# Optimization experiments

Measured on AMD Instinct MI355X. Metric: run time of the kernel, lower is better.

## Reference

```python
import jax, jax.numpy as jnp
import numpy as np

# (multiplicity, dim=2l+1) per irreducible field, for both input and output
RS = [(8, 1), (8, 3), (8, 5)]
SIZE = 3          # conv kernel spatial size
B_EL = 2          # radial basis elements per (i,j) kernel block
EPS = 1e-5


def _se3_bn_conv(x, weight, bases):
    """Training-mode SE3BatchNorm stats fused into dynamic kernel build + conv3d.
    x: (B, C_in, D, H, W); weight: flat (sum mi*mj*b_el,);
    bases[i][j]: (b_el, di, dj, SIZE, SIZE, SIZE).
    """
    B = x.shape[0]
    means = []    # per scalar (d==1) field: (m,)
    scales = []   # per field: (m,) inverse-std factors
    ix = 0
    for m, d in RS:
        field = x[:, ix:ix + m * d].reshape(B, m, d, -1)
        ix += m * d
        if d == 1:
            mean = jax.lax.stop_gradient(field.mean(axis=-1).mean(axis=0).reshape(-1))
            field = field - mean.reshape(1, m, 1, 1)
            means.append(mean)
        # reduce='mean': sum over d, mean over spatial, mean over batch (detached)
        norm = jax.lax.stop_gradient(jnp.sum(field * field, axis=2).mean(axis=-1).mean(axis=0))
        scales.append((norm + EPS) ** -0.5)

    # Build normalized dynamic kernel blocks and compensating bias
    widx = 0
    row_blocks = []
    bias_parts = []
    for i, (mi, di) in enumerate(RS):
        col_blocks = []
        bia = jnp.zeros((mi * di,), x.dtype)
        imean = 0
        for j, (mj, dj) in enumerate(RS):
            basis = bases[i][j]                     # (b, di, dj, s, s, s)
            b = basis.shape[0]
            w = weight[widx:widx + mi * mj * b].reshape(mi, mj, b)
            widx += mi * mj * b
            w = w * scales[j][None, :, None]        # per-input-field BN rescale
            # block: (mi*di, mj*dj, s, s, s)
            block = jnp.einsum('uvb,bdexyz->udvexyz', w, basis)
            col_blocks.append(block.reshape(mi * di, mj * dj, SIZE, SIZE, SIZE))
            if di == 1 and dj == 1:
                mean = means[imean]
                imean += 1
                identity = basis.reshape(b, -1).sum(-1)         # (b,)
                corr = (w.reshape(-1, b) @ identity[:, None]).reshape(mi, mj)
                bia = bia - (corr @ mean[:, None]).reshape(-1)
        row_blocks.append(jnp.concatenate(col_blocks, axis=1))
        bias_parts.append(bia)
    kernel = jnp.concatenate(row_blocks, axis=0)    # (C_out, C_in, s, s, s)
    bias = jnp.concatenate(bias_parts)              # (C_out,)

    out = jax.lax.conv_general_dilated(
        x, kernel, window_strides=(1, 1, 1), padding='VALID',
        dimension_numbers=('NCDHW', 'OIDHW', 'NCDHW'))
    return out + bias[None, :, None, None, None]


def setup_inputs() -> dict:
    key = jax.random.key(0)
    k_x, k_w = jax.random.split(key)
    C = sum(m * d for m, d in RS)  # 72
    x = jax.random.normal(k_x, (8, C, 32, 32, 32), jnp.float32)
    total_w = sum(mi * mj * B_EL for mi, _ in RS for mj, _ in RS)  # 1152
    weight = jax.random.normal(k_w, (total_w,), jnp.float32) * 0.1
    inp = {'x': x, 'weight': weight}
    for i, (mi, di) in enumerate(RS):
        for j, (mj, dj) in enumerate(RS):
            kb = jax.random.fold_in(key, 100 + 10 * i + j)
            inp['basis_{}_{}'.format(i, j)] = jax.random.normal(
                kb, (B_EL, di, dj, SIZE, SIZE, SIZE), jnp.float32) / (SIZE ** 1.5)
    return inp


def reference(x, weight, basis_0_0, basis_0_1, basis_0_2,
              basis_1_0, basis_1_1, basis_1_2,
              basis_2_0, basis_2_1, basis_2_2):
    bases = [[basis_0_0, basis_0_1, basis_0_2],
             [basis_1_0, basis_1_1, basis_1_2],
             [basis_2_0, basis_2_1, basis_2_2]]
    return _se3_bn_conv(x, weight, bases)
```

## Files before the change

kernel.cpp:

```cpp
#include <hip/hip_runtime.h>
#include <hip/hip_fp16.h>
#include <math.h>

#define NCH 72
#define SP  32768
#define NBATCH 8
#define NTOT (NBATCH*SP)

#define WS_SUMX   0
#define WS_SUMSQ  72
#define WS_SCALE  144
#define WS_BIAS   216
#define WS_K      288

#define WS_XH_BYTES 323712
#define XH_ROW   2720
#define XH_PLANE 87040
#define XH_BATCH 2785280

typedef __attribute__((ext_vector_type(8))) _Float16 half8;
typedef __attribute__((ext_vector_type(4))) float float4v;
typedef __attribute__((ext_vector_type(4))) int int4v;

__device__ __forceinline__ void chmap(int c, int& f, int& m, int& d, int& dim) {
  if (c < 8)       { f = 0; m = c;          d = 0;          dim = 1; }
  else if (c < 32) { f = 1; m = (c - 8)/3;  d = (c - 8)%3;  dim = 3; }
  else             { f = 2; m = (c - 32)/5; d = (c - 32)%5; dim = 5; }
}

__global__ __launch_bounds__(256) void prepack_kernel(const float* __restrict__ x,
                                                      float* __restrict__ ws) {
  __shared__ __align__(16) short tile[256 * 88];
  __shared__ float segS[72][3], segQ[72][3];
  const int t    = threadIdx.x;
  const int z    = blockIdx.x >> 1;
  const int half = blockIdx.x & 1;
  const int b    = blockIdx.y;
  ushort* xh = (ushort*)((char*)ws + WS_XH_BYTES);
  const float* xb = x + (size_t)b * NCH * SP + z * 1024 + half * 512;

  const int ci_s = t % 72, seg = t / 72;
  float accS = 0.f, accQ = 0.f;

  *(int4v*)&tile[t * 88 + 72] = (int4v){0, 0, 0, 0};

  for (int c = 0; c < 2; ++c) {
    if (c) __syncthreads();
    #pragma unroll
    for (int cig = 0; cig < 18; ++cig) {
      float v0 = xb[(size_t)(cig*4 + 0) * SP + c * 256 + t];
      float v1 = xb[(size_t)(cig*4 + 1) * SP + c * 256 + t];
      float v2 = xb[(size_t)(cig*4 + 2) * SP + c * 256 + t];
      float v3 = xb[(size_t)(cig*4 + 3) * SP + c * 256 + t];
      short s4[4] = { (short)__half_as_short(__float2half(v0)),
                      (short)__half_as_short(__float2half(v1)),
                      (short)__half_as_short(__float2half(v2)),
                      (short)__half_as_short(__float2half(v3)) };
      *(int2*)&tile[t * 88 + cig * 4] = *(const int2*)s4;
    }
    __syncthreads();
    {
      ushort* gb = xh + (size_t)b * XH_BATCH + (size_t)(z * 32 + (half * 2 + c) * 8) * XH_ROW;
      #pragma unroll
      for (int j = 0; j < 10; ++j) {
        const int s   = t + j * 256;
        const int pos = s / 10, part = s - pos * 10;
        const int4v v = *(const int4v*)&tile[pos * 88 + part * 8];
        const int row = pos >> 5, xx = pos & 31;
        *(int4v*)(gb + (size_t)row * XH_ROW + xx * 80 + part * 8) = v;
      }
    }
    if (seg < 3) {
      const int p0 = seg * 86;
      const int pn = (seg == 2) ? 84 : 86;
      for (int i = 0; i < pn; ++i) {
        const float v = __half2float(__short_as_half(tile[(p0 + i) * 88 + ci_s]));
        accS += v; accQ += v * v;
      }
    }
  }
  if (seg < 3) { segS[ci_s][seg] = accS; segQ[ci_s][seg] = accQ; }
  __syncthreads();
  if (t < 144) {
    const int which = t / 72, ci = t % 72;
    const float v = which ? (segQ[ci][0] + segQ[ci][1] + segQ[ci][2])
                          : (segS[ci][0] + segS[ci][1] + segS[ci][2]);
    atomicAdd(&ws[(which ? WS_SUMSQ : WS_SUMX) + ci], v);
  }
}

__global__ __launch_bounds__(128) void finalize_kernel(const float* __restrict__ weight,
                                                       const float* __restrict__ basis00,
                                                       float* __restrict__ ws) {
  __shared__ float s_mean[8], s_scale[8];
  const int c = threadIdx.x;
  const float invN = 1.0f / (float)NTOT;
  if (c < NCH) {
    float norm;
    if (c < 8) {
      float m = ws[WS_SUMX + c] * invN;
      norm = ws[WS_SUMSQ + c] * invN - m * m;
      s_mean[c] = m;
    } else if (c < 32) {
      int m0 = 8 + ((c - 8) / 3) * 3;
      norm = (ws[WS_SUMSQ+m0] + ws[WS_SUMSQ+m0+1] + ws[WS_SUMSQ+m0+2]) * invN;
    } else {
      int m0 = 32 + ((c - 32) / 5) * 5;
      norm = (ws[WS_SUMSQ+m0] + ws[WS_SUMSQ+m0+1] + ws[WS_SUMSQ+m0+2]
            + ws[WS_SUMSQ+m0+3] + ws[WS_SUMSQ+m0+4]) * invN;
    }
    float sc = 1.0f / sqrtf(norm + 1e-5f);
    ws[WS_SCALE + c] = sc;
    if (c < 8) s_scale[c] = sc;
  }
  __syncthreads();
  if (c < NCH) {
    float bia = 0.f;
    if (c < 8) {
      float id0 = 0.f, id1 = 0.f;
      #pragma unroll
      for (int t = 0; t < 27; ++t) { id0 += basis00[t]; id1 += basis00[27 + t]; }
      #pragma unroll
      for (int v = 0; v < 8; ++v) {
        float s  = s_scale[v];
        float w0 = weight[(c*8 + v)*2 + 0] * s;
        float w1 = weight[(c*8 + v)*2 + 1] * s;
        bia -= (w0 * id0 + w1 * id1) * s_mean[v];
      }
    }
    ws[WS_BIAS + c] = bia;
  }
}

__global__ __launch_bounds__(256) void build_half_kernel(const float* __restrict__ weight,
    float* __restrict__ ws,
    const float* __restrict__ b00, const float* __restrict__ b01, const float* __restrict__ b02,
    const float* __restrict__ b10, const float* __restrict__ b11, const float* __restrict__ b12,
    const float* __restrict__ b20, const float* __restrict__ b21, const float* __restrict__ b22) {
  const int tid = blockIdx.x * 256 + threadIdx.x;
  if (tid >= 315 * 512) return;
  const int blk = tid >> 9;
  const int e   = tid & 511;
  const int tap = blk / 35;
  const int r   = blk - tap * 35;
  const int kc  = r / 5, cj = r - (r / 5) * 5;
  const int l   = e >> 3, j = e & 7;
  const int co  = cj * 16 + (l & 15);
  const int kk  = kc * 32 + ((l >> 4) << 3) + j;
  short val = 0;
  if (co < NCH && kk < 216) {
    const int dx = kk / 72, ci = kk - dx * 72;
    int fi, u, dd, di; chmap(co, fi, u, dd, di);
    int fj, v, ee, dj; chmap(ci, fj, v, ee, dj);
    const float* bs[9] = {b00, b01, b02, b10, b11, b12, b20, b21, b22};
    const float* basis = bs[fi * 3 + fj];
    const float sc = ws[WS_SCALE + ci];
    const float* wp = weight + (fi * 3 + fj) * 128 + (u * 8 + v) * 2;
    const float w0 = wp[0] * sc, w1 = wp[1] * sc;
    const int t = tap * 3 + dx;
    const float f = w0 * basis[(dd * dj + ee) * 27 + t]
                  + w1 * basis[((di + dd) * dj + ee) * 27 + t];
    val = __half_as_short(__float2half(f));
  }
  ((short*)(ws + WS_K))[tid] = val;
}

__global__ __launch_bounds__(128, 2) void conv_direct(const float* __restrict__ ws,
                                                      float* __restrict__ out) {
  const int lane = threadIdx.x & 63;
  const int wv   = threadIdx.x >> 6;
  const int lx   = lane & 15;
  const int q    = lane >> 4;
  const int i  = blockIdx.x;
  const int b  = i & 7;
  const int qq = i >> 3;
  const int yp = qq % 15;
  const int zp = qq / 15;
  const int y  = yp * 2 + wv;
  const int zb = zp * 2;

  const char* xhb = (const char*)ws + WS_XH_BYTES + (size_t)b * (XH_BATCH * 2);
  const char* Kb  = (const char*)(ws + WS_K);
  const float* __restrict__ bias = ws + WS_BIAS;

  const int lb16 = lane * 16;

  float4v acc[2][2][5];
  #pragma unroll
  for (int sz = 0; sz < 2; ++sz)
    #pragma unroll
    for (int s = 0; s < 2; ++s)
      #pragma unroll
      for (int cj = 0; cj < 5; ++cj)
        acc[sz][s][cj] = (float4v){0.f, 0.f, 0.f, 0.f};

#define LOADG(T, A, Bf) {                                                         \
    const int t_   = (T);                                                         \
    const int tap_ = t_ / 7;                                                      \
    const int kc_  = t_ - tap_ * 7;                                               \
    const int dz_  = tap_ / 3, dy_ = tap_ - 3 * dz_;                              \
    const char* r0_ = xhb + (size_t)(((zb + dz_) * 32) + (y + dy_)) * (XH_ROW*2); \
    const char* r1_ = r0_ + (XH_PLANE * 2);                                       \
    const char* bk_ = Kb + (size_t)tap_ * (35*1024) + (size_t)kc_ * (5*1024) + lb16; \
    const int kk0_ = kc_ * 32 + (q << 3);                                         \
    const int dx_  = (kk0_ >= 144) ? 2 : ((kk0_ >= 72) ? 1 : 0);                  \
    const int ao_  = (lx * 80 + kk0_ + 8 * dx_) * 2;                              \
    Bf[0] = *(const half8*)(bk_);                                                 \
    Bf[1] = *(const half8*)(bk_ + 1024);                                          \
    Bf[2] = *(const half8*)(bk_ + 2048);                                          \
    Bf[3] = *(const half8*)(bk_ + 3072);                                          \
    Bf[4] = *(const half8*)(bk_ + 4096);                                          \
    A[0] = *(const half8*)(r0_ + ao_);                                            \
    A[1] = *(const half8*)(r0_ + ao_ + 2560);                                     \
    A[2] = *(const half8*)(r1_ + ao_);                                            \
    A[3] = *(const half8*)(r1_ + ao_ + 2560);                                     \
  }

#define MF1(A, Bf, CJ)                                                                         \
    acc[0][0][CJ] = __builtin_amdgcn_mfma_f32_16x16x32_f16(A[0], Bf[CJ], acc[0][0][CJ], 0,0,0); \
    acc[0][1][CJ] = __builtin_amdgcn_mfma_f32_16x16x32_f16(A[1], Bf[CJ], acc[0][1][CJ], 0,0,0); \
    acc[1][0][CJ] = __builtin_amdgcn_mfma_f32_16x16x32_f16(A[2], Bf[CJ], acc[1][0][CJ], 0,0,0); \
    acc[1][1][CJ] = __builtin_amdgcn_mfma_f32_16x16x32_f16(A[3], Bf[CJ], acc[1][1][CJ], 0,0,0);

#define MFMAG(A, Bf) {                       \
    __builtin_amdgcn_s_setprio(1);           \
    MF1(A, Bf, 0) MF1(A, Bf, 1)              \
    MF1(A, Bf, 2) MF1(A, Bf, 3)              \
    MF1(A, Bf, 4)                            \
    __builtin_amdgcn_s_setprio(0);           \
  }

  half8 A0[4], B0[5], A1[4], B1[5];
  LOADG(0, A0, B0);
  #pragma unroll 1
  for (int t = 0; t < 62; t += 2) {
    LOADG(t + 1, A1, B1);
    MFMAG(A0, B0);
    LOADG(t + 2, A0, B0);
    MFMAG(A1, B1);
  }
  MFMAG(A0, B0);

#undef LOADG
#undef MF1
#undef MFMAG

  #pragma unroll
  for (int cj = 0; cj < 5; ++cj) {
    const int co = cj * 16 + lx;
    if (co < NCH) {
      const float bv = bias[co];
      #pragma unroll
      for (int sz = 0; sz < 2; ++sz) {
        float* ob = out + ((size_t)(b * NCH + co) * 30 + (zb + sz)) * 900 + y * 30;
        #pragma unroll
        for (int s = 0; s < 2; ++s) {
          const int x0 = s * 16 + q * 4;
          const float4v v = acc[sz][s][cj];
          float2 p0; p0.x = v[0] + bv; p0.y = v[1] + bv;
          *(float2*)(ob + x0) = p0;
          if (x0 + 2 < 30) {
            float2 p1; p1.x = v[2] + bv; p1.y = v[3] + bv;
            *(float2*)(ob + x0 + 2) = p1;
          }
        }
      }
    }
  }
}

extern "C" void kernel_launch(void* const* d_in, const int* in_sizes, int n_in,
                              void* d_out, int out_size, void* d_ws, size_t ws_size,
                              hipStream_t stream) {
  const float* x = (const float*)d_in[0];
  const float* w = (const float*)d_in[1];
  const float* bs[9];
  for (int i = 0; i < 9; ++i) bs[i] = (const float*)d_in[2 + i];
  float* ws  = (float*)d_ws;
  float* out = (float*)d_out;

  hipMemsetAsync(d_ws, 0, 144 * sizeof(float), stream);

  prepack_kernel<<<dim3(64, NBATCH), 256, 0, stream>>>(x, ws);
  finalize_kernel<<<1, 128, 0, stream>>>(w, bs[0], ws);
  build_half_kernel<<<(315 * 512 + 255) / 256, 256, 0, stream>>>(
      w, ws, bs[0], bs[1], bs[2], bs[3], bs[4], bs[5], bs[6], bs[7], bs[8]);
  conv_direct<<<dim3(1800), 128, 0, stream>>>(ws, out);
}
```

Baseline: 285.8 us.

## Fold finalize into kernel build and triple-buffer conv fragment loads

The separate single-block finalize kernel is removed. Each build thread now recomputes its input channel's BN scale from the raw sums, and block 0 also computes the scalar-field bias, which saves one kernel launch. Independently, the conv main loop moves from double to triple buffering of A/B fragments, so loads run one more step ahead of the MFMA groups. That adds roughly 36 more VGPRs per thread under a launch bound of 2 blocks per CU, which risks spills or lower occupancy.

```diff
diff --git a/kernel.cpp b/kernel.cpp
--- a/kernel.cpp
+++ b/kernel.cpp
@@ -89,80 +89,78 @@
   }
 }
 
-__global__ __launch_bounds__(128) void finalize_kernel(const float* __restrict__ weight,
-                                                       const float* __restrict__ basis00,
-                                                       float* __restrict__ ws) {
-  __shared__ float s_mean[8], s_scale[8];
-  const int c = threadIdx.x;
-  const float invN = 1.0f / (float)NTOT;
-  if (c < NCH) {
-    float norm;
-    if (c < 8) {
-      float m = ws[WS_SUMX + c] * invN;
-      norm = ws[WS_SUMSQ + c] * invN - m * m;
-      s_mean[c] = m;
-    } else if (c < 32) {
-      int m0 = 8 + ((c - 8) / 3) * 3;
-      norm = (ws[WS_SUMSQ+m0] + ws[WS_SUMSQ+m0+1] + ws[WS_SUMSQ+m0+2]) * invN;
-    } else {
-      int m0 = 32 + ((c - 32) / 5) * 5;
-      norm = (ws[WS_SUMSQ+m0] + ws[WS_SUMSQ+m0+1] + ws[WS_SUMSQ+m0+2]
-            + ws[WS_SUMSQ+m0+3] + ws[WS_SUMSQ+m0+4]) * invN;
-    }
-    float sc = 1.0f / sqrtf(norm + 1e-5f);
-    ws[WS_SCALE + c] = sc;
-    if (c < 8) s_scale[c] = sc;
-  }
-  __syncthreads();
-  if (c < NCH) {
-    float bia = 0.f;
-    if (c < 8) {
-      float id0 = 0.f, id1 = 0.f;
-      #pragma unroll
-      for (int t = 0; t < 27; ++t) { id0 += basis00[t]; id1 += basis00[27 + t]; }
-      #pragma unroll
-      for (int v = 0; v < 8; ++v) {
-        float s  = s_scale[v];
-        float w0 = weight[(c*8 + v)*2 + 0] * s;
-        float w1 = weight[(c*8 + v)*2 + 1] * s;
-        bia -= (w0 * id0 + w1 * id1) * s_mean[v];
-      }
-    }
-    ws[WS_BIAS + c] = bia;
-  }
-}
-
 __global__ __launch_bounds__(256) void build_half_kernel(const float* __restrict__ weight,
     float* __restrict__ ws,
     const float* __restrict__ b00, const float* __restrict__ b01, const float* __restrict__ b02,
     const float* __restrict__ b10, const float* __restrict__ b11, const float* __restrict__ b12,
     const float* __restrict__ b20, const float* __restrict__ b21, const float* __restrict__ b22) {
   const int tid = blockIdx.x * 256 + threadIdx.x;
-  if (tid >= 315 * 512) return;
-  const int blk = tid >> 9;
-  const int e   = tid & 511;
-  const int tap = blk / 35;
-  const int r   = blk - tap * 35;
-  const int kc  = r / 5, cj = r - (r / 5) * 5;
-  const int l   = e >> 3, j = e & 7;
-  const int co  = cj * 16 + (l & 15);
-  const int kk  = kc * 32 + ((l >> 4) << 3) + j;
-  short val = 0;
-  if (co < NCH && kk < 216) {
-    const int dx = kk / 72, ci = kk - dx * 72;
-    int fi, u, dd, di; chmap(co, fi, u, dd, di);
-    int fj, v, ee, dj; chmap(ci, fj, v, ee, dj);
-    const float* bs[9] = {b00, b01, b02, b10, b11, b12, b20, b21, b22};
-    const float* basis = bs[fi * 3 + fj];
-    const float sc = ws[WS_SCALE + ci];
-    const float* wp = weight + (fi * 3 + fj) * 128 + (u * 8 + v) * 2;
-    const float w0 = wp[0] * sc, w1 = wp[1] * sc;
-    const int t = tap * 3 + dx;
-    const float f = w0 * basis[(dd * dj + ee) * 27 + t]
-                  + w1 * basis[((di + dd) * dj + ee) * 27 + t];
-    val = __half_as_short(__float2half(f));
-  }
-  ((short*)(ws + WS_K))[tid] = val;
+  const float invN = 1.0f / (float)NTOT;
+  if (tid < 315 * 512) {
+    const int blk = tid >> 9;
+    const int e   = tid & 511;
+    const int tap = blk / 35;
+    const int r   = blk - tap * 35;
+    const int kc  = r / 5, cj = r - (r / 5) * 5;
+    const int l   = e >> 3, j = e & 7;
+    const int co  = cj * 16 + (l & 15);
+    const int kk  = kc * 32 + ((l >> 4) << 3) + j;
+    short val = 0;
+    if (co < NCH && kk < 216) {
+      const int dx = kk / 72, ci = kk - dx * 72;
+      int fi, u, dd, di; chmap(co, fi, u, dd, di);
+      int fj, v, ee, dj; chmap(ci, fj, v, ee, dj);
+      const float* bs[9] = {b00, b01, b02, b10, b11, b12, b20, b21, b22};
+      const float* basis = bs[fi * 3 + fj];
+      float norm;
+      if (ci < 8) {
+        float m = ws[WS_SUMX + ci] * invN;
+        norm = ws[WS_SUMSQ + ci] * invN - m * m;
+      } else if (ci < 32) {
+        int m0 = 8 + ((ci - 8) / 3) * 3;
+        norm = (ws[WS_SUMSQ+m0] + ws[WS_SUMSQ+m0+1] + ws[WS_SUMSQ+m0+2]) * invN;
+      } else {
+        int m0 = 32 + ((ci - 32) / 5) * 5;
+        norm = (ws[WS_SUMSQ+m0] + ws[WS_SUMSQ+m0+1] + ws[WS_SUMSQ+m0+2]
+              + ws[WS_SUMSQ+m0+3] + ws[WS_SUMSQ+m0+4]) * invN;
+      }
+      const float sc = 1.0f / sqrtf(norm + 1e-5f);
+      const float* wp = weight + (fi * 3 + fj) * 128 + (u * 8 + v) * 2;
+      const float w0 = wp[0] * sc, w1 = wp[1] * sc;
+      const int t = tap * 3 + dx;
+      const float f = w0 * basis[(dd * dj + ee) * 27 + t]
+                    + w1 * basis[((di + dd) * dj + ee) * 27 + t];
+      val = __half_as_short(__float2half(f));
+    }
+    ((short*)(ws + WS_K))[tid] = val;
+  }
+  if (blockIdx.x == 0) {
+    __shared__ float s_mean[8], s_scale[8];
+    const int c = threadIdx.x;
+    if (c < 8) {
+      float m = ws[WS_SUMX + c] * invN;
+      float norm = ws[WS_SUMSQ + c] * invN - m * m;
+      s_mean[c]  = m;
+      s_scale[c] = 1.0f / sqrtf(norm + 1e-5f);
+    }
+    __syncthreads();
+    if (c < NCH) {
+      float bia = 0.f;
+      if (c < 8) {
+        float id0 = 0.f, id1 = 0.f;
+        #pragma unroll
+        for (int t = 0; t < 27; ++t) { id0 += b00[t]; id1 += b00[27 + t]; }
+        #pragma unroll
+        for (int v = 0; v < 8; ++v) {
+          float s  = s_scale[v];
+          float w0 = weight[(c*8 + v)*2 + 0] * s;
+          float w1 = weight[(c*8 + v)*2 + 1] * s;
+          bia -= (w0 * id0 + w1 * id1) * s_mean[v];
+        }
+      }
+      ws[WS_BIAS + c] = bia;
+    }
+  }
 }
 
 __global__ __launch_bounds__(128, 2) void conv_direct(const float* __restrict__ ws,
@@ -230,16 +228,22 @@
     __builtin_amdgcn_s_setprio(0);           \
   }
 
-  half8 A0[4], B0[5], A1[4], B1[5];
+  half8 A0[4], B0[5], A1[4], B1[5], A2[4], B2[5];
   LOADG(0, A0, B0);
+  LOADG(1, A1, B1);
   #pragma unroll 1
-  for (int t = 0; t < 62; t += 2) {
-    LOADG(t + 1, A1, B1);
+  for (int t = 0; t < 60; t += 3) {
+    LOADG(t + 2, A2, B2);
     MFMAG(A0, B0);
-    LOADG(t + 2, A0, B0);
+    LOADG(t + 3, A0, B0);
     MFMAG(A1, B1);
-  }
+    LOADG(t + 4, A1, B1);
+    MFMAG(A2, B2);
+  }
+  LOADG(62, A2, B2);
   MFMAG(A0, B0);
+  MFMAG(A1, B1);
+  MFMAG(A2, B2);
 
 #undef LOADG
 #undef MF1
@@ -282,7 +286,6 @@
   hipMemsetAsync(d_ws, 0, 144 * sizeof(float), stream);
 
   prepack_kernel<<<dim3(64, NBATCH), 256, 0, stream>>>(x, ws);
-  finalize_kernel<<<1, 128, 0, stream>>>(w, bs[0], ws);
   build_half_kernel<<<(315 * 512 + 255) / 256, 256, 0, stream>>>(
       w, ws, bs[0], bs[1], bs[2], bs[3], bs[4], bs[5], bs[6], bs[7], bs[8]);
   conv_direct<<<dim3(1800), 128, 0, stream>>>(ws, out);
```

Measured after the change: 281.0 us. No clear change (-1.7%).
